# Performance work log

Measured on AMD Instinct MI355X. Metric: run time of the kernel, lower is better.

Reference implementation:

```python
import jax, jax.numpy as jnp
import numpy as np

SMOOTH = 1.0      # self.smooth
NUM_ITER = 10     # iter_
EPS = 1e-07
INF = 1e12        # stand-in for +inf in squared-distance init


def _maxpool(x, window):
    # torch max_pool3d(stride=1, padding=w//2): pad with -inf, window max
    pads = ((0, 0), (0, 0)) + tuple((w // 2, w // 2) for w in window)
    return jax.lax.reduce_window(x, -jnp.inf, jax.lax.max, (1, 1) + window, (1, 1, 1, 1, 1), pads)


def _soft_erode(x):  # x: [B,1,D,H,W]
    p1 = -_maxpool(-x, (3, 1, 1))
    p2 = -_maxpool(-x, (1, 3, 1))
    p3 = -_maxpool(-x, (1, 1, 3))
    return jnp.minimum(jnp.minimum(p1, p2), p3)


def _soft_open(x):
    return _maxpool(_soft_erode(x), (3, 3, 3))  # dilate(erode(x))


def _soft_skel(x, n_iter):
    skel = jax.nn.relu(x - _soft_open(x))
    for _ in range(n_iter):
        x = _soft_erode(x)
        delta = jax.nn.relu(x - _soft_open(x))
        skel = skel + jax.nn.relu(delta - skel * delta)
    return skel


def _edt_pass(d2, axis):
    # 1D squared-distance min-convolution: out[i] = min_j (i-j)^2 + d2[j]
    L = d2.shape[axis]
    d2m = jnp.moveaxis(d2, axis, -1)                 # [..., L]
    i = jnp.arange(L, dtype=d2.dtype)
    sq = (i[:, None] - i[None, :]) ** 2              # [L, L]
    out = jnp.min(d2m[..., None, :] + sq, axis=-1)   # [..., L]
    return jnp.moveaxis(out, -1, axis)


def _edt(mask):
    # exact Euclidean distance transform: distance of nonzero voxels to nearest zero voxel
    d2 = jnp.where(mask > 0, INF, 0.0).astype(jnp.float32)  # [B,D,H,W]
    for ax in (1, 2, 3):
        d2 = _edt_pass(d2, ax)
    return jnp.sqrt(d2)


def _get_weights(mask, skel):
    # mask, skel: [B,D,H,W] binary float
    dist = _edt(mask)
    dist = jnp.where(mask == 0, 0.0, dist)
    on_skel = skel == 1
    skel_r = jnp.where(on_skel, dist, 0.0)
    rmax = jnp.max(skel_r.reshape(skel_r.shape[0], -1), axis=1).reshape(-1, 1, 1, 1)
    valid = rmax > 0
    rmax_safe = jnp.where(valid, rmax, 1.0)
    dist_n = jnp.where(valid, dist / rmax_safe, dist)
    skel_rn = jnp.where(valid, skel_r / rmax_safe, skel_r)
    # dim == 3 branch: skel_1_R2_norm
    skel_1r2 = jnp.where(on_skel, (1.0 + EPS) / (skel_rn ** 2 + EPS), 0.0)
    return dist_n, skel_rn, skel_1r2


def _combine(A, B, C):
    # D = B*C, overwritten by A*C where (A != 0) & (B == 0)
    return jnp.where((A != 0) & (B == 0), A * C, B * C)


def reference(y_pred, y_true):
    # y_pred: [B,C,D,H,W] logits; y_true: [B,1,D,H,W] int labels
    fore = jnp.max(y_pred[:, 1:], axis=1, keepdims=True)
    logits = jnp.concatenate([y_pred[:, :1], fore], axis=1)   # [B,2,D,H,W]
    prob = jax.nn.softmax(logits, axis=1)
    yp = (prob[:, 1] > 0.5).astype(jnp.float32)               # [B,D,H,W]
    yt = (y_true > 0).astype(jnp.float32)[:, 0]               # [B,D,H,W]

    skel_p = _soft_skel(yp[:, None], NUM_ITER)[:, 0]
    skel_t = _soft_skel(yt[:, None], NUM_ITER)[:, 0]

    q_vl, q_slvl, q_sl = _get_weights(yt, skel_t)
    q_vp, q_spvp, q_sp = _get_weights(yp, skel_p)

    w_tprec = (jnp.sum(q_sp * q_vl) + SMOOTH) / (jnp.sum(_combine(q_spvp, q_slvl, q_sp)) + SMOOTH)
    w_tsens = (jnp.sum(q_sl * q_vp) + SMOOTH) / (jnp.sum(_combine(q_slvl, q_spvp, q_sl)) + SMOOTH)
    return 1.0 - 2.0 * (w_tprec * w_tsens) / (w_tprec + w_tsens)


def setup_inputs() -> dict:
    key = jax.random.key(0)
    k1, k2 = jax.random.split(key)
    y_pred = jax.random.normal(k1, (2, 2, 64, 96, 96), dtype=jnp.float32)
    y_true = jax.random.randint(k2, (2, 1, 64, 96, 96), 0, 2, dtype=jnp.int32)
    return {"y_pred": y_pred, "y_true": y_true}
```

## Files before the change

### kernel.cpp

```cpp
#include <hip/hip_runtime.h>

namespace {

constexpr int Bn = 2;
constexpr int Dn = 64;
constexpr int Hn = 96;
constexpr int Wn = 96;
constexpr int HW = Hn * Wn;
constexpr int S  = Dn * HW;
constexpr int NBS = Bn * S;
constexpr int NT  = 2 * NBS;
constexpr int WPP = HW / 32;
constexpr int WPS = S / 32;
constexpr int NTW = NT / 32;
constexpr float EPSf = 1e-7f;
constexpr int BLK_SUMS = NBS / 4 / 256;
#define BIGF 1e12f
constexpr int LINF = 1 << 20;

__global__ __launch_bounds__(256) void k_bin0(const float* __restrict__ logits,
                                              const int* __restrict__ labels,
                                              unsigned short* __restrict__ FZ,
                                              unsigned char* __restrict__ DZ) {
  __shared__ unsigned bits[64];
  __shared__ unsigned zlo[32], zhi[32];
  int slab = blockIdx.x / 288;
  int cg = blockIdx.x - slab * 288;
  int c0 = cg * 32;
  int tid = threadIdx.x;
  int lane = tid & 63;
  for (int t = tid; t < 2048; t += 256) {
    int zz = t >> 5;
    int col = t & 31;
    int s = zz * HW + c0 + col;
    bool v;
    if (slab < 2) {
      float l0 = logits[(slab * 2 + 0) * S + s];
      float l1 = logits[(slab * 2 + 1) * S + s];
      v = l1 > l0;
    } else {
      v = labels[(slab - 2) * S + s] > 0;
    }
    unsigned long long m = __ballot(v);
    if (lane == 0)       bits[zz] = (unsigned)m;
    else if (lane == 32) bits[zz] = (unsigned)(m >> 32);
  }
  __syncthreads();
  if (tid < 64) {
    int col = tid & 31;
    int base = (tid < 32) ? 0 : 32;
    unsigned zw = 0u;
    #pragma unroll
    for (int j = 0; j < 32; ++j)
      zw |= (((bits[base + j] >> col) & 1u) ^ 1u) << j;
    if (tid < 32) zlo[col] = zw; else zhi[col] = zw;
  }
  __syncthreads();
  int col = tid & 31;
  int chunk = tid >> 5;
  int i0 = chunk * 8;
  unsigned long long Z = ((unsigned long long)zhi[col] << 32) | (unsigned long long)zlo[col];
  unsigned short* o = FZ + slab * S + c0 + col;
  unsigned char* o1 = DZ + slab * S + c0 + col;
  #pragma unroll
  for (int s = 0; s < 8; ++s) {
    int i = i0 + s;
    unsigned long long below = Z & ((2ull << i) - 1ull);
    unsigned long long above = Z >> i;
    unsigned short fv;
    unsigned char dv;
    if (below | above) {
      int ddn = below ? (i - (63 - __builtin_clzll(below))) : 99;
      int dup = above ? __builtin_ctzll(above) : 99;
      int d = ddn < dup ? ddn : dup;
      fv = (unsigned short)(d * d);
      dv = (unsigned char)d;
    } else {
      fv = 0xFFFFu;
      dv = 255;
    }
    o[i * HW] = fv;
    o1[i * HW] = dv;
  }
}

__global__ __launch_bounds__(256) void k_edtl1(const unsigned short* __restrict__ FZ,
                                               const unsigned char* __restrict__ DZ,
                                               float* __restrict__ EF,
                                               unsigned char* __restrict__ D1) {
  __shared__ __align__(16) unsigned shm[8640];
  unsigned short* fz = (unsigned short*)shm;
  unsigned char*  dz = (unsigned char*)(shm + 4608);
  unsigned char*  t1 = (unsigned char*)(shm + 6912);
  unsigned short* o1 = (unsigned short*)(shm + 7488);
  unsigned short* Afwd = (unsigned short*)shm;
  unsigned short* Bbwd = (unsigned short*)(shm + 4608);
  int slab = blockIdx.x >> 8;
  int z = (blockIdx.x >> 2) & 63;
  int y0 = (blockIdx.x & 3) * 24;
  int tid = threadIdx.x;
  int pb = slab * S + z * HW;
  {
    const uint4* s4 = (const uint4*)(FZ + pb);
    uint4* d4 = (uint4*)fz;
    for (int t = tid; t < 1152; t += 256) d4[t] = s4[t];
    const uint4* s2 = (const uint4*)(DZ + pb);
    uint4* d2 = (uint4*)(shm + 4608);
    for (int t = tid; t < 576; t += 256) d2[t] = s2[t];
  }
  __syncthreads();
  if (tid < 96) {
    int xx = tid;
    int P = LINF;
    int A[24];
    for (int j = 0; j < y0; ++j) {
      int v = dz[j * 96 + xx]; if (v == 255) v = LINF;
      P = min(P, v - j);
    }
    #pragma unroll
    for (int s = 0; s < 24; ++s) {
      int j = y0 + s;
      int v = dz[j * 96 + xx]; if (v == 255) v = LINF;
      P = min(P, v - j);
      A[s] = j + P;
    }
    int Sv = LINF;
    for (int j = 95; j >= y0 + 24; --j) {
      int v = dz[j * 96 + xx]; if (v == 255) v = LINF;
      Sv = min(Sv, v + j);
    }
    #pragma unroll
    for (int s = 23; s >= 0; --s) {
      int j = y0 + s;
      int v = dz[j * 96 + xx]; if (v == 255) v = LINF;
      Sv = min(Sv, v + j);
      int t = min(A[s], Sv - j);
      t1[s * 96 + xx] = (unsigned char)(t > 254 ? 255 : t);
    }
  }
  __syncthreads();
  for (int v = tid; v < 2304; v += 256) {
    int rr = v / 96;
    int xx = v - rr * 96;
    int y = y0 + rr;
    int r = t1[rr * 96 + xx];
    unsigned short res;
    if (r == 255) {
      res = 0xFFFFu;
    } else {
      int lo = y - r; if (lo < 0) lo = 0;
      int hi = y + r; if (hi > 95) hi = 95;
      int best = 1 << 30;
      for (int j = lo; j <= hi; ++j) {
        unsigned short f = fz[j * 96 + xx];
        if (f != 0xFFFFu) {
          int dd = y - j;
          best = min(best, dd * dd + (int)f);
        }
      }
      res = (unsigned short)best;
    }
    o1[rr * 96 + xx] = res;
  }
  __syncthreads();
  if (tid < 24) {
    int rr = tid;
    int P = LINF;
    for (int j = 0; j < 96; ++j) {
      int v = t1[rr * 96 + j]; if (v == 255) v = LINF;
      P = min(P, v - j);
      int a = j + P;
      Afwd[rr * 96 + j] = (unsigned short)(a > 60000 ? 60000 : a);
    }
  }
  if (tid >= 64 && tid < 88) {
    int rr = tid - 64;
    int Sv = LINF;
    for (int j = 95; j >= 0; --j) {
      int v = t1[rr * 96 + j]; if (v == 255) v = LINF;
      Sv = min(Sv, v + j);
      int b = Sv - j;
      Bbwd[rr * 96 + j] = (unsigned short)(b > 60000 ? 60000 : b);
    }
  }
  __syncthreads();
  for (int v = tid; v < 2304; v += 256) {
    int rr = v / 96;
    int x = v - rr * 96;
    int d1v = min((int)Afwd[rr * 96 + x], (int)Bbwd[rr * 96 + x]);
    float outf;
    int d1c;
    if (d1v > 253) {
      outf = BIGF;
      d1c = 12;
    } else {
      d1c = d1v < 12 ? d1v : 12;
      int lo = x - d1v; if (lo < 0) lo = 0;
      int hi = x + d1v; if (hi > 95) hi = 95;
      int best = 1 << 30;
      for (int j = lo; j <= hi; ++j) {
        unsigned short f = o1[rr * 96 + j];
        if (f != 0xFFFFu) {
          int dd = x - j;
          best = min(best, dd * dd + (int)f);
        }
      }
      outf = (float)best;
    }
    int gb = pb + (y0 + rr) * 96 + x;
    EF[gb] = outf;
    D1[gb] = (unsigned char)d1c;
  }
}

__global__ __launch_bounds__(256) void k_skelmax(const unsigned char* __restrict__ D1,
                                                 const float* __restrict__ EF,
                                                 unsigned* __restrict__ SKELB,
                                                 float* __restrict__ pmax) {
  __shared__ unsigned char zm[26 * 96];
  __shared__ unsigned char cen[26 * 96];
  __shared__ float ldsf[4];
  int slab = blockIdx.x >> 8;
  int z = (blockIdx.x >> 2) & 63;
  int y0 = (blockIdx.x & 3) * 24;
  int tid = threadIdx.x;
  int pb = slab * S + z * HW;
  for (int t = tid; t < 2496; t += 256) {
    int rr = t / 96;
    int x = t - rr * 96;
    int yy = y0 - 1 + rr;
    unsigned char m = 0, cv = 0;
    if (yy >= 0 && yy < Hn) {
      int base = slab * S + yy * 96 + x;
      cv = D1[base + z * HW];
      m = cv;
      if (z > 0) { unsigned char a = D1[base + (z - 1) * HW]; m = m > a ? m : a; }
      if (z < Dn - 1) { unsigned char a = D1[base + (z + 1) * HW]; m = m > a ? m : a; }
    }
    zm[t] = m;
    cen[t] = cv;
  }
  __syncthreads();
  float mm = 0.0f;
  int wbase = slab * WPS + z * WPP + y0 * 3;
  int lane = tid & 63;
  #pragma unroll
  for (int round = 0; round < 9; ++round) {
    int v = round * 256 + tid;
    int rr = v / 96;
    int x = v - rr * 96;
    int b1 = rr * 96 + x;
    unsigned char mx = zm[b1];
    { unsigned char a = zm[b1 + 96]; mx = mx > a ? mx : a; }
    { unsigned char a = zm[b1 + 192]; mx = mx > a ? mx : a; }
    if (x > 0) {
      unsigned char a0 = zm[b1 - 1], a1 = zm[b1 + 95], a2 = zm[b1 + 191];
      unsigned char a = a0 > a1 ? a0 : a1; a = a > a2 ? a : a2;
      mx = mx > a ? mx : a;
    }
    if (x < Wn - 1) {
      unsigned char a0 = zm[b1 + 1], a1 = zm[b1 + 97], a2 = zm[b1 + 193];
      unsigned char a = a0 > a1 ? a0 : a1; a = a > a2 ? a : a2;
      mx = mx > a ? mx : a;
    }
    unsigned char d1 = cen[b1 + 96];
    bool sk = (d1 == mx) && (d1 >= 1) && (d1 <= 11);
    unsigned long long bal = __ballot(sk);
    if (lane == 0)       SKELB[wbase + (v >> 5)] = (unsigned)bal;
    else if (lane == 32) SKELB[wbase + (v >> 5)] = (unsigned)(bal >> 32);
    if (sk) mm = fmaxf(mm, EF[pb + (y0 + rr) * 96 + x]);
  }
  #pragma unroll
  for (int o = 32; o > 0; o >>= 1) mm = fmaxf(mm, __shfl_xor(mm, o, 64));
  if (lane == 0) ldsf[tid >> 6] = mm;
  __syncthreads();
  if (tid == 0)
    pmax[blockIdx.x] = fmaxf(fmaxf(ldsf[0], ldsf[1]), fmaxf(ldsf[2], ldsf[3]));
}

__global__ __launch_bounds__(256) void k_sums(const float* __restrict__ d2,
                                              const unsigned* __restrict__ skel,
                                              const float* __restrict__ pmax,
                                              double* __restrict__ ps) {
  __shared__ float lmax[4];
  __shared__ double ldsd[4][4];
  int tid = threadIdx.x;
  {
    int wave = tid >> 6, lane = tid & 63;
    const float* pw = pmax + wave * 256;
    float v = fmaxf(fmaxf(pw[lane], pw[lane + 64]),
                    fmaxf(pw[lane + 128], pw[lane + 192]));
    #pragma unroll
    for (int o = 32; o > 0; o >>= 1) v = fmaxf(v, __shfl_xor(v, o, 64));
    if (lane == 0) lmax[wave] = v;
  }
  __syncthreads();
  int q = blockIdx.x * 256 + tid;
  int idx0 = q * 4;
  int b = idx0 / S;
  float rmax_p = sqrtf(lmax[b]);
  float rmax_t = sqrtf(lmax[2 + b]);
  float4 dp4 = ((const float4*)d2)[q];
  float4 dt4 = ((const float4*)(d2 + NBS))[q];
  unsigned spw = (skel[idx0 >> 5] >> (idx0 & 31)) & 0xFu;
  unsigned stw = (skel[(NBS + idx0) >> 5] >> (idx0 & 31)) & 0xFu;
  const float* dp = &dp4.x;
  const float* dt = &dt4.x;
  double acc[4] = {0.0, 0.0, 0.0, 0.0};
  #pragma unroll
  for (int s = 0; s < 4; ++s) {
    float dist_p = sqrtf(dp[s]);
    float dist_t = sqrtf(dt[s]);
    bool sp = (spw >> s) & 1u;
    bool st = (stw >> s) & 1u;
    float q_vp = (rmax_p > 0.0f) ? dist_p / rmax_p : dist_p;
    float q_vl = (rmax_t > 0.0f) ? dist_t / rmax_t : dist_t;
    float q_spvp = sp ? q_vp : 0.0f;
    float q_slvl = st ? q_vl : 0.0f;
    float q_sp = sp ? (1.0f + EPSf) / (q_spvp * q_spvp + EPSf) : 0.0f;
    float q_sl = st ? (1.0f + EPSf) / (q_slvl * q_slvl + EPSf) : 0.0f;
    acc[0] += (double)(q_sp * q_vl);
    acc[1] += (double)(((q_spvp != 0.0f) && (q_slvl == 0.0f)) ? q_spvp * q_sp
                                                              : q_slvl * q_sp);
    acc[2] += (double)(q_sl * q_vp);
    acc[3] += (double)(((q_slvl != 0.0f) && (q_spvp == 0.0f)) ? q_slvl * q_sl
                                                              : q_spvp * q_sl);
  }
  #pragma unroll
  for (int k = 0; k < 4; ++k)
    #pragma unroll
    for (int o = 32; o > 0; o >>= 1)
      acc[k] += __shfl_xor(acc[k], o, 64);
  if ((tid & 63) == 0) {
    #pragma unroll
    for (int k = 0; k < 4; ++k) ldsd[tid >> 6][k] = acc[k];
  }
  __syncthreads();
  if (tid == 0) {
    #pragma unroll
    for (int k = 0; k < 4; ++k)
      ps[blockIdx.x * 4 + k] = ldsd[0][k] + ldsd[1][k] + ldsd[2][k] + ldsd[3][k];
  }
}

__global__ __launch_bounds__(256) void k_final(const double* __restrict__ ps,
                                               float* __restrict__ out) {
  __shared__ double ldsd[4][4];
  int tid = threadIdx.x;
  double s[4] = {0.0, 0.0, 0.0, 0.0};
  for (int i = tid; i < BLK_SUMS; i += 256) {
    s[0] += ps[i * 4 + 0];
    s[1] += ps[i * 4 + 1];
    s[2] += ps[i * 4 + 2];
    s[3] += ps[i * 4 + 3];
  }
  #pragma unroll
  for (int k = 0; k < 4; ++k)
    #pragma unroll
    for (int o = 32; o > 0; o >>= 1)
      s[k] += __shfl_xor(s[k], o, 64);
  if ((tid & 63) == 0) {
    #pragma unroll
    for (int k = 0; k < 4; ++k) ldsd[tid >> 6][k] = s[k];
  }
  __syncthreads();
  if (tid == 0) {
    double tot[4];
    #pragma unroll
    for (int k = 0; k < 4; ++k)
      tot[k] = ldsd[0][k] + ldsd[1][k] + ldsd[2][k] + ldsd[3][k];
    double wp = (tot[0] + 1.0) / (tot[1] + 1.0);
    double ws = (tot[2] + 1.0) / (tot[3] + 1.0);
    out[0] = (float)(1.0 - 2.0 * (wp * ws) / (wp + ws));
  }
}

}

extern "C" void kernel_launch(void* const* d_in, const int* in_sizes, int n_in,
                              void* d_out, int out_size, void* d_ws, size_t ws_size,
                              hipStream_t stream) {
  (void)in_sizes; (void)n_in; (void)out_size; (void)ws_size;
  const float* logits = (const float*)d_in[0];
  const int* labels   = (const int*)d_in[1];
  float* out = (float*)d_out;

  float* EF = (float*)d_ws;
  unsigned short* FZ = (unsigned short*)(EF + NT);
  unsigned char* DZ  = (unsigned char*)(FZ + NT);
  unsigned char* D1  = DZ + NT;
  unsigned* SKELB = (unsigned*)(D1 + NT);
  float* PMAX  = (float*)(SKELB + NTW);
  double* PS   = (double*)(PMAX + 1024);

  k_bin0<<<1152, 256, 0, stream>>>(logits, labels, FZ, DZ);
  k_edtl1<<<1024, 256, 0, stream>>>(FZ, DZ, EF, D1);
  k_skelmax<<<1024, 256, 0, stream>>>(D1, EF, SKELB, PMAX);
  k_sums<<<1152, 256, 0, stream>>>(EF, SKELB, PMAX, PS);
  k_final<<<1, 256, 0, stream>>>(PS, out);
}
```

Baseline: 118.6 us.

## Fuse EDT and skeleton-max kernels, recompute neighbor-slice distances in LDS

Merges the distance-transform kernel with the skeleton/max kernel. Each block now loads three z-slices of the byte distance field and recomputes the L1 chamfer distances for the neighbouring slices and rows in shared memory, so the D1 buffer and its global round trip are gone. The 16-bit squared-distance buffer is dropped as well, and squares are computed from the byte distance. This saves one launch and a lot of global traffic. In exchange it does redundant per-slice work, and the larger shared-memory footprint (about 49 KB) may lower occupancy.

```diff
diff --git a/kernel.cpp b/kernel.cpp
--- a/kernel.cpp
+++ b/kernel.cpp
@@ -20,7 +20,6 @@
 
 __global__ __launch_bounds__(256) void k_bin0(const float* __restrict__ logits,
                                               const int* __restrict__ labels,
-                                              unsigned short* __restrict__ FZ,
                                               unsigned char* __restrict__ DZ) {
   __shared__ unsigned bits[64];
   __shared__ unsigned zlo[32], zhi[32];
@@ -60,82 +59,90 @@
   int chunk = tid >> 5;
   int i0 = chunk * 8;
   unsigned long long Z = ((unsigned long long)zhi[col] << 32) | (unsigned long long)zlo[col];
-  unsigned short* o = FZ + slab * S + c0 + col;
   unsigned char* o1 = DZ + slab * S + c0 + col;
   #pragma unroll
   for (int s = 0; s < 8; ++s) {
     int i = i0 + s;
     unsigned long long below = Z & ((2ull << i) - 1ull);
     unsigned long long above = Z >> i;
-    unsigned short fv;
     unsigned char dv;
     if (below | above) {
       int ddn = below ? (i - (63 - __builtin_clzll(below))) : 99;
       int dup = above ? __builtin_ctzll(above) : 99;
       int d = ddn < dup ? ddn : dup;
-      fv = (unsigned short)(d * d);
       dv = (unsigned char)d;
     } else {
-      fv = 0xFFFFu;
       dv = 255;
     }
-    o[i * HW] = fv;
     o1[i * HW] = dv;
   }
 }
 
-__global__ __launch_bounds__(256) void k_edtl1(const unsigned short* __restrict__ FZ,
-                                               const unsigned char* __restrict__ DZ,
-                                               float* __restrict__ EF,
-                                               unsigned char* __restrict__ D1) {
-  __shared__ __align__(16) unsigned shm[8640];
-  unsigned short* fz = (unsigned short*)shm;
-  unsigned char*  dz = (unsigned char*)(shm + 4608);
-  unsigned char*  t1 = (unsigned char*)(shm + 6912);
-  unsigned short* o1 = (unsigned short*)(shm + 7488);
-  unsigned short* Afwd = (unsigned short*)shm;
-  unsigned short* Bbwd = (unsigned short*)(shm + 4608);
+__global__ __launch_bounds__(256) void k_edtskel(const unsigned char* __restrict__ DZ,
+                                                 float* __restrict__ EF,
+                                                 unsigned* __restrict__ SKELB,
+                                                 float* __restrict__ pmax) {
+  __shared__ __align__(16) unsigned char shm[49760];
+  unsigned char* dzl = shm;
+  unsigned char* t1l = shm + 27648;
+  unsigned char* d1l = shm + 35136;
+  unsigned short* o1 = (unsigned short*)(shm + 42624);
+  unsigned char* zm  = shm + 47232;
+  float* ldsf = (float*)(shm + 49744);
   int slab = blockIdx.x >> 8;
   int z = (blockIdx.x >> 2) & 63;
   int y0 = (blockIdx.x & 3) * 24;
   int tid = threadIdx.x;
   int pb = slab * S + z * HW;
-  {
-    const uint4* s4 = (const uint4*)(FZ + pb);
-    uint4* d4 = (uint4*)fz;
-    for (int t = tid; t < 1152; t += 256) d4[t] = s4[t];
-    const uint4* s2 = (const uint4*)(DZ + pb);
-    uint4* d2 = (uint4*)(shm + 4608);
-    for (int t = tid; t < 576; t += 256) d2[t] = s2[t];
-  }
-  __syncthreads();
-  if (tid < 96) {
-    int xx = tid;
+  for (int t = tid; t < 1728; t += 256) {
+    int p = t / 576;
+    int idx = t - p * 576;
+    int zp = z - 1 + p;
+    uint4 val;
+    if (zp >= 0 && zp < Dn)
+      val = ((const uint4*)(DZ + slab * S + zp * HW))[idx];
+    else
+      val = make_uint4(0xFFFFFFFFu, 0xFFFFFFFFu, 0xFFFFFFFFu, 0xFFFFFFFFu);
+    ((uint4*)dzl)[t] = val;
+  }
+  __syncthreads();
+  for (int task = tid; task < 288; task += 256) {
+    int p = task / 96;
+    int xx = task - p * 96;
+    int zp = z - 1 + p;
+    if (zp < 0 || zp >= Dn) continue;
+    const unsigned char* dzp = dzl + p * HW;
     int P = LINF;
-    int A[24];
-    for (int j = 0; j < y0; ++j) {
-      int v = dz[j * 96 + xx]; if (v == 255) v = LINF;
+    int A[26];
+    for (int j = 0; j < y0 - 1; ++j) {
+      int v = dzp[j * 96 + xx]; if (v == 255) v = LINF;
       P = min(P, v - j);
     }
     #pragma unroll
-    for (int s = 0; s < 24; ++s) {
-      int j = y0 + s;
-      int v = dz[j * 96 + xx]; if (v == 255) v = LINF;
-      P = min(P, v - j);
-      A[s] = j + P;
+    for (int s = 0; s < 26; ++s) {
+      int j = y0 - 1 + s;
+      if (j >= 0 && j < 96) {
+        int v = dzp[j * 96 + xx]; if (v == 255) v = LINF;
+        P = min(P, v - j);
+        A[s] = j + P;
+      } else A[s] = LINF;
     }
     int Sv = LINF;
-    for (int j = 95; j >= y0 + 24; --j) {
-      int v = dz[j * 96 + xx]; if (v == 255) v = LINF;
+    for (int j = 95; j >= y0 + 25; --j) {
+      int v = dzp[j * 96 + xx]; if (v == 255) v = LINF;
       Sv = min(Sv, v + j);
     }
     #pragma unroll
-    for (int s = 23; s >= 0; --s) {
-      int j = y0 + s;
-      int v = dz[j * 96 + xx]; if (v == 255) v = LINF;
-      Sv = min(Sv, v + j);
-      int t = min(A[s], Sv - j);
-      t1[s * 96 + xx] = (unsigned char)(t > 254 ? 255 : t);
+    for (int s = 25; s >= 0; --s) {
+      int j = y0 - 1 + s;
+      int t = 255;
+      if (j >= 0 && j < 96) {
+        int v = dzp[j * 96 + xx]; if (v == 255) v = LINF;
+        Sv = min(Sv, v + j);
+        int tv = min(A[s], Sv - j);
+        t = tv > 254 ? 255 : tv;
+      }
+      t1l[p * 2496 + s * 96 + xx] = (unsigned char)t;
     }
   }
   __syncthreads();
@@ -143,7 +150,7 @@
     int rr = v / 96;
     int xx = v - rr * 96;
     int y = y0 + rr;
-    int r = t1[rr * 96 + xx];
+    int r = t1l[1 * 2496 + (rr + 1) * 96 + xx];
     unsigned short res;
     if (r == 255) {
       res = 0xFFFFu;
@@ -151,55 +158,74 @@
       int lo = y - r; if (lo < 0) lo = 0;
       int hi = y + r; if (hi > 95) hi = 95;
       int best = 1 << 30;
+      const unsigned char* dzc = dzl + 1 * HW + xx;
       for (int j = lo; j <= hi; ++j) {
-        unsigned short f = fz[j * 96 + xx];
-        if (f != 0xFFFFu) {
+        int dv = dzc[j * 96];
+        if (dv != 255) {
           int dd = y - j;
-          best = min(best, dd * dd + (int)f);
+          best = min(best, dd * dd + dv * dv);
         }
       }
       res = (unsigned short)best;
     }
     o1[rr * 96 + xx] = res;
   }
-  __syncthreads();
-  if (tid < 24) {
-    int rr = tid;
+  for (int task = tid; task < 78; task += 256) {
+    int p = task / 26;
+    int rr = task - p * 26;
+    int zp = z - 1 + p;
+    int yy = y0 - 1 + rr;
+    unsigned char* drow = d1l + p * 2496 + rr * 96;
+    if (zp < 0 || zp >= Dn || yy < 0 || yy >= Hn) {
+      for (int j = 0; j < 96; ++j) drow[j] = 0;
+      continue;
+    }
+    const unsigned char* trow = t1l + p * 2496 + rr * 96;
     int P = LINF;
     for (int j = 0; j < 96; ++j) {
-      int v = t1[rr * 96 + j]; if (v == 255) v = LINF;
+      int v = trow[j]; if (v == 255) v = LINF;
       P = min(P, v - j);
       int a = j + P;
-      Afwd[rr * 96 + j] = (unsigned short)(a > 60000 ? 60000 : a);
-    }
-  }
-  if (tid >= 64 && tid < 88) {
-    int rr = tid - 64;
+      drow[j] = (unsigned char)(a > 254 ? 255 : a);
+    }
     int Sv = LINF;
     for (int j = 95; j >= 0; --j) {
-      int v = t1[rr * 96 + j]; if (v == 255) v = LINF;
+      int v = trow[j]; if (v == 255) v = LINF;
       Sv = min(Sv, v + j);
       int b = Sv - j;
-      Bbwd[rr * 96 + j] = (unsigned short)(b > 60000 ? 60000 : b);
-    }
-  }
-  __syncthreads();
-  for (int v = tid; v < 2304; v += 256) {
+      int f = drow[j];
+      int d = min(f, b > 254 ? 255 : b);
+      drow[j] = (unsigned char)d;
+    }
+  }
+  __syncthreads();
+  for (int t = tid; t < 2496; t += 256) {
+    int a0 = min((int)d1l[t], 12);
+    int a1 = min((int)d1l[2496 + t], 12);
+    int a2 = min((int)d1l[4992 + t], 12);
+    int m = a0 > a1 ? a0 : a1;
+    zm[t] = (unsigned char)(m > a2 ? m : a2);
+  }
+  __syncthreads();
+  float mm = 0.0f;
+  int wbase = slab * WPS + z * WPP + y0 * 3;
+  int lane = tid & 63;
+  #pragma unroll
+  for (int round = 0; round < 9; ++round) {
+    int v = round * 256 + tid;
     int rr = v / 96;
     int x = v - rr * 96;
-    int d1v = min((int)Afwd[rr * 96 + x], (int)Bbwd[rr * 96 + x]);
+    int d1v = d1l[1 * 2496 + (rr + 1) * 96 + x];
     float outf;
-    int d1c;
-    if (d1v > 253) {
+    if (d1v == 255) {
       outf = BIGF;
-      d1c = 12;
     } else {
-      d1c = d1v < 12 ? d1v : 12;
       int lo = x - d1v; if (lo < 0) lo = 0;
       int hi = x + d1v; if (hi > 95) hi = 95;
       int best = 1 << 30;
+      const unsigned short* orow = o1 + rr * 96;
       for (int j = lo; j <= hi; ++j) {
-        unsigned short f = o1[rr * 96 + j];
+        unsigned short f = orow[j];
         if (f != 0xFFFFu) {
           int dd = x - j;
           best = min(best, dd * dd + (int)f);
@@ -207,68 +233,27 @@
       }
       outf = (float)best;
     }
-    int gb = pb + (y0 + rr) * 96 + x;
-    EF[gb] = outf;
-    D1[gb] = (unsigned char)d1c;
-  }
-}
-
-__global__ __launch_bounds__(256) void k_skelmax(const unsigned char* __restrict__ D1,
-                                                 const float* __restrict__ EF,
-                                                 unsigned* __restrict__ SKELB,
-                                                 float* __restrict__ pmax) {
-  __shared__ unsigned char zm[26 * 96];
-  __shared__ unsigned char cen[26 * 96];
-  __shared__ float ldsf[4];
-  int slab = blockIdx.x >> 8;
-  int z = (blockIdx.x >> 2) & 63;
-  int y0 = (blockIdx.x & 3) * 24;
-  int tid = threadIdx.x;
-  int pb = slab * S + z * HW;
-  for (int t = tid; t < 2496; t += 256) {
-    int rr = t / 96;
-    int x = t - rr * 96;
-    int yy = y0 - 1 + rr;
-    unsigned char m = 0, cv = 0;
-    if (yy >= 0 && yy < Hn) {
-      int base = slab * S + yy * 96 + x;
-      cv = D1[base + z * HW];
-      m = cv;
-      if (z > 0) { unsigned char a = D1[base + (z - 1) * HW]; m = m > a ? m : a; }
-      if (z < Dn - 1) { unsigned char a = D1[base + (z + 1) * HW]; m = m > a ? m : a; }
-    }
-    zm[t] = m;
-    cen[t] = cv;
-  }
-  __syncthreads();
-  float mm = 0.0f;
-  int wbase = slab * WPS + z * WPP + y0 * 3;
-  int lane = tid & 63;
-  #pragma unroll
-  for (int round = 0; round < 9; ++round) {
-    int v = round * 256 + tid;
-    int rr = v / 96;
-    int x = v - rr * 96;
-    int b1 = rr * 96 + x;
-    unsigned char mx = zm[b1];
+    int b1 = (rr + 1) * 96 + x;
+    unsigned char mx = zm[b1 - 96];
+    { unsigned char a = zm[b1]; mx = mx > a ? mx : a; }
     { unsigned char a = zm[b1 + 96]; mx = mx > a ? mx : a; }
-    { unsigned char a = zm[b1 + 192]; mx = mx > a ? mx : a; }
     if (x > 0) {
-      unsigned char a0 = zm[b1 - 1], a1 = zm[b1 + 95], a2 = zm[b1 + 191];
+      unsigned char a0 = zm[b1 - 97], a1 = zm[b1 - 1], a2 = zm[b1 + 95];
       unsigned char a = a0 > a1 ? a0 : a1; a = a > a2 ? a : a2;
       mx = mx > a ? mx : a;
     }
     if (x < Wn - 1) {
-      unsigned char a0 = zm[b1 + 1], a1 = zm[b1 + 97], a2 = zm[b1 + 193];
+      unsigned char a0 = zm[b1 - 95], a1 = zm[b1 + 1], a2 = zm[b1 + 97];
       unsigned char a = a0 > a1 ? a0 : a1; a = a > a2 ? a : a2;
       mx = mx > a ? mx : a;
     }
-    unsigned char d1 = cen[b1 + 96];
-    bool sk = (d1 == mx) && (d1 >= 1) && (d1 <= 11);
+    int d1c = min(d1v, 12);
+    bool sk = (d1c == (int)mx) && (d1c >= 1) && (d1c <= 11);
     unsigned long long bal = __ballot(sk);
     if (lane == 0)       SKELB[wbase + (v >> 5)] = (unsigned)bal;
     else if (lane == 32) SKELB[wbase + (v >> 5)] = (unsigned)(bal >> 32);
-    if (sk) mm = fmaxf(mm, EF[pb + (y0 + rr) * 96 + x]);
+    if (sk) mm = fmaxf(mm, outf);
+    EF[pb + (y0 + rr) * 96 + x] = outf;
   }
   #pragma unroll
   for (int o = 32; o > 0; o >>= 1) mm = fmaxf(mm, __shfl_xor(mm, o, 64));
@@ -386,16 +371,13 @@
   float* out = (float*)d_out;
 
   float* EF = (float*)d_ws;
-  unsigned short* FZ = (unsigned short*)(EF + NT);
-  unsigned char* DZ  = (unsigned char*)(FZ + NT);
-  unsigned char* D1  = DZ + NT;
-  unsigned* SKELB = (unsigned*)(D1 + NT);
+  unsigned char* DZ  = (unsigned char*)(EF + NT);
+  unsigned* SKELB = (unsigned*)(DZ + NT);
   float* PMAX  = (float*)(SKELB + NTW);
   double* PS   = (double*)(PMAX + 1024);
 
-  k_bin0<<<1152, 256, 0, stream>>>(logits, labels, FZ, DZ);
-  k_edtl1<<<1024, 256, 0, stream>>>(FZ, DZ, EF, D1);
-  k_skelmax<<<1024, 256, 0, stream>>>(D1, EF, SKELB, PMAX);
+  k_bin0<<<1152, 256, 0, stream>>>(logits, labels, DZ);
+  k_edtskel<<<1024, 256, 0, stream>>>(DZ, EF, SKELB, PMAX);
   k_sums<<<1152, 256, 0, stream>>>(EF, SKELB, PMAX, PS);
   k_final<<<1, 256, 0, stream>>>(PS, out);
 }
```

Measured after the change: 138.1 us. 1.17x slower.
